# Kernel optimization log

Hardware: AMD Instinct MI355X
Metric: run time of the kernel (lower is better)

The kernel has to match this reference:

```python
import jax, jax.numpy as jnp
import numpy as np

FP8_MAX = 448.0   # max finite value of float8_e4m3fn
GROUP = 128       # quant group size (both act cols and weight blocks)


def fp8_roundtrip(v):
    # Round-to-nearest onto the fp8 e4m3fn grid, back to f32.
    return v.astype(jnp.float8_e4m3fn).astype(jnp.float32)


def setup_inputs() -> dict:
    key = jax.random.key(0)
    k1, k2, k3 = jax.random.split(key, 3)
    M, H = 8192, 4096
    x = jax.random.normal(k1, (M, 2 * H), dtype=jnp.float32)
    # weight: rand -> fp8 grid (stored as f32 values lying exactly on fp8 grid)
    w_q = fp8_roundtrip(jax.random.uniform(k2, (H, H), dtype=jnp.float32))
    # per-(128,128)-block weight scales
    wscale = jax.random.uniform(k3, (H // GROUP, H // GROUP), dtype=jnp.float32)
    return {"x": x, "w_q": w_q, "wscale": wscale}


def reference(x, w_q, wscale):
    H = x.shape[-1] // 2
    # SiluAndMul: silu(gate) * up
    y = jax.nn.silu(x[:, :H]) * x[:, H:]            # [M, H]
    M = y.shape[0]
    # --- activation group quant, group shape (1, 128) ---
    g = y.reshape(M, H // GROUP, GROUP)
    amax = jnp.max(jnp.abs(g), axis=-1, keepdims=True)
    scale = jnp.maximum(amax, 1e-12) / FP8_MAX      # [M, H/128, 1]
    q = fp8_roundtrip(g / scale)                    # fp8-grid values
    y_dq = (q * scale).reshape(M, H)                # dequantized activation
    # --- weight block dequant, block shape (128, 128) ---
    nk, nn = H // GROUP, H // GROUP
    w_dq = (w_q.reshape(nk, GROUP, nn, GROUP) * wscale[:, None, :, None]).reshape(H, H)
    # block-fp8 linear: out[m, n] = sum_k y_dq[m, k] * w_dq[k, n]
    return y_dq @ w_dq
```

## Files before the change

kernel.cpp:

```cpp
#include <hip/hip_runtime.h>
#include <hip/hip_fp8.h>

#define MDIM 8192
#define HDIM 4096

typedef float f32x4 __attribute__((ext_vector_type(4)));
typedef long i64;

__device__ inline void gload_lds16(const void* g, void* l) {
  __builtin_amdgcn_global_load_lds(
      (const __attribute__((address_space(1))) void*)g,
      (__attribute__((address_space(3))) void*)l, 16, 0, 0);
}

__global__ __launch_bounds__(256) void silu_quant_kernel(
    const float* __restrict__ x, unsigned char* __restrict__ q,
    float* __restrict__ st) {
  const int m = blockIdx.x;
  const int t = threadIdx.x;
  const int g = t >> 3;
  const int i = t & 7;
  const float* xr = x + (size_t)m * (2 * HDIM);

  float v[16];
  float amax = 0.f;
#pragma unroll
  for (int j = 0; j < 4; ++j) {
    const int off = g * 128 + j * 32 + i * 4;
    f32x4 gate = *(const f32x4*)(xr + off);
    f32x4 up = *(const f32x4*)(xr + HDIM + off);
#pragma unroll
    for (int c = 0; c < 4; ++c) {
      float gg = gate[c];
      float s = gg / (1.f + expf(-gg));
      float val = s * up[c];
      v[j * 4 + c] = val;
      amax = fmaxf(amax, fabsf(val));
    }
  }
#pragma unroll
  for (int d = 1; d < 8; d <<= 1) amax = fmaxf(amax, __shfl_xor(amax, d, 64));
  const float scale = fmaxf(amax, 1e-12f) / 448.0f;

#pragma unroll
  for (int j = 0; j < 4; ++j) {
    unsigned int pk = 0;
#pragma unroll
    for (int c = 0; c < 4; ++c) {
      __hip_fp8_e4m3 qv(v[j * 4 + c] / scale);
      pk |= ((unsigned int)qv.__x) << (8 * c);
    }
    *(unsigned int*)(q + (size_t)m * HDIM + g * 128 + j * 32 + i * 4) = pk;
  }
  if (i == 0) st[(size_t)g * MDIM + m] = scale;
}

__global__ __launch_bounds__(256) void wconv_kernel(
    const float* __restrict__ w, unsigned char* __restrict__ wt) {
  __shared__ __align__(16) unsigned char tile[64 * 68];
  const int t = threadIdx.x;
  const int n0 = (blockIdx.x & 63) * 64;
  const int k0 = (blockIdx.x >> 6) * 64;
  {
    const int r = t >> 4;
    const int c4 = (t & 15) << 2;
#pragma unroll
    for (int j = 0; j < 4; ++j) {
      const int kr = r + j * 16;
      f32x4 vv = *(const f32x4*)(w + (size_t)(k0 + kr) * HDIM + n0 + c4);
      unsigned int pk = 0;
#pragma unroll
      for (int c = 0; c < 4; ++c) {
        __hip_fp8_e4m3 qv(vv[c]);
        pk |= ((unsigned int)qv.__x) << (8 * c);
      }
      *(unsigned int*)(tile + kr * 68 + c4) = pk;
    }
  }
  __syncthreads();
  {
    const int n = t >> 4;
    const int k4 = (t & 15) << 2;
#pragma unroll
    for (int j = 0; j < 4; ++j) {
      const int nn = n + j * 16;
      unsigned int pk = 0;
#pragma unroll
      for (int c = 0; c < 4; ++c)
        pk |= ((unsigned int)tile[(k4 + c) * 68 + nn]) << (8 * c);
      *(unsigned int*)(wt + (size_t)(n0 + nn) * HDIM + k0 + k4) = pk;
    }
  }
}

__global__ __launch_bounds__(256, 2) void gemm_fp8_kernel(
    const unsigned char* __restrict__ Aq,
    const unsigned char* __restrict__ Bt,
    const float* __restrict__ st,
    const float* __restrict__ wsc,
    float* __restrict__ out) {
  __shared__ __align__(16) unsigned char As[128 * 128];
  __shared__ __align__(16) unsigned char Bs[128 * 128];
  __shared__ __align__(16) float sas[128];

  const int t = threadIdx.x;
  const int ntile = blockIdx.x & 31;
  const int mtile = blockIdx.x >> 5;
  const int m0 = mtile * 128, n0 = ntile * 128;

  const int l = t & 63, wid = t >> 6;
  const int wm = wid >> 1, wn = wid & 1;
  const int lrow = l & 15, lhi = l >> 4;

  f32x4 acc[4][4];
#pragma unroll
  for (int a = 0; a < 4; ++a)
#pragma unroll
    for (int b = 0; b < 4; ++b) acc[a][b] = (f32x4){0.f, 0.f, 0.f, 0.f};

  const int sr = t >> 3;
  const int skc = (t & 7) ^ (sr & 7);

  for (int kb = 0; kb < 32; ++kb) {
    __syncthreads();
    const int kbase = kb * 128 + skc * 16;
#pragma unroll
    for (int p = 0; p < 4; ++p) {
      const int row = sr + p * 32;
      gload_lds16(Aq + (size_t)(m0 + row) * HDIM + kbase, As + (p * 256 + t) * 16);
      gload_lds16(Bt + (size_t)(n0 + row) * HDIM + kbase, Bs + (p * 256 + t) * 16);
    }
    if (t < 128) sas[t] = st[(size_t)kb * MDIM + m0 + t];
    __syncthreads();

    const float sw = wsc[kb * 32 + ntile];

    f32x4 blk[4][4];
#pragma unroll
    for (int kk = 0; kk < 4; ++kk) {
      const int kbyte = kk * 32 + lhi * 8;
      const int chunk = (((kbyte >> 4) ^ (lrow & 7)) << 4) + (kbyte & 15);
      i64 af[4], bf[4];
#pragma unroll
      for (int mi = 0; mi < 4; ++mi) {
        const int row = wm * 64 + mi * 16 + lrow;
        af[mi] = *(const i64*)(As + row * 128 + chunk);
      }
#pragma unroll
      for (int ni = 0; ni < 4; ++ni) {
        const int row = wn * 64 + ni * 16 + lrow;
        bf[ni] = *(const i64*)(Bs + row * 128 + chunk);
      }
#pragma unroll
      for (int mi = 0; mi < 4; ++mi)
#pragma unroll
        for (int ni = 0; ni < 4; ++ni) {
          f32x4 cin = (kk == 0) ? (f32x4){0.f, 0.f, 0.f, 0.f} : blk[mi][ni];
          blk[mi][ni] =
              __builtin_amdgcn_mfma_f32_16x16x32_fp8_fp8(af[mi], bf[ni], cin, 0, 0, 0);
        }
    }
#pragma unroll
    for (int mi = 0; mi < 4; ++mi) {
      f32x4 sa = *(const f32x4*)(sas + wm * 64 + mi * 16 + lhi * 4);
      f32x4 sm;
#pragma unroll
      for (int r = 0; r < 4; ++r) sm[r] = sa[r] * sw;
#pragma unroll
      for (int ni = 0; ni < 4; ++ni)
#pragma unroll
        for (int r = 0; r < 4; ++r)
          acc[mi][ni][r] = fmaf(blk[mi][ni][r], sm[r], acc[mi][ni][r]);
    }
  }

#pragma unroll
  for (int mi = 0; mi < 4; ++mi)
#pragma unroll
    for (int r = 0; r < 4; ++r) {
      const int grow = m0 + wm * 64 + mi * 16 + lhi * 4 + r;
      float* orow = out + (size_t)grow * HDIM + n0 + wn * 64 + lrow;
#pragma unroll
      for (int ni = 0; ni < 4; ++ni) orow[ni * 16] = acc[mi][ni][r];
    }
}

extern "C" void kernel_launch(void* const* d_in, const int* in_sizes, int n_in,
                              void* d_out, int out_size, void* d_ws, size_t ws_size,
                              hipStream_t stream) {
  const float* x = (const float*)d_in[0];
  const float* wq = (const float*)d_in[1];
  const float* wsc = (const float*)d_in[2];
  float* out = (float*)d_out;

  unsigned char* q = (unsigned char*)d_ws;
  unsigned char* wt = q + (size_t)MDIM * HDIM;
  float* st = (float*)(wt + (size_t)HDIM * HDIM);

  silu_quant_kernel<<<MDIM, 256, 0, stream>>>(x, q, st);
  wconv_kernel<<<(HDIM / 64) * (HDIM / 64), 256, 0, stream>>>(wq, wt);
  gemm_fp8_kernel<<<(MDIM / 128) * (HDIM / 128), 256, 0, stream>>>(q, wt, st, wsc, out);
}
```

Baseline: 341.6 us.

## Switch GEMM to bf16 with pre-dequantized operands and double-buffered 256x256 tiles

Activations are now quantized to the fp8 grid, dequantized, and stored as bf16. Weights are pre-multiplied by their block scales and stored as bf16. This removes the per-k-block scale epilogue from the GEMM, which becomes a plain bf16 MFMA kernel with 256x256 tiles, 512 threads, double-buffered LDS staging and a swizzled block order. The trade-off is that bf16 MFMA has lower throughput than fp8 and the operands take twice the memory traffic. Rounding the dequantized values to bf16 may also add a small error against the reference.

```diff
diff --git a/kernel.cpp b/kernel.cpp
--- a/kernel.cpp
+++ b/kernel.cpp
@@ -1,11 +1,14 @@
 #include <hip/hip_runtime.h>
 #include <hip/hip_fp8.h>
+#include <hip/hip_bf16.h>
 
 #define MDIM 8192
 #define HDIM 4096
+#define NKT 64
 
 typedef float f32x4 __attribute__((ext_vector_type(4)));
-typedef long i64;
+typedef short bf16x8 __attribute__((ext_vector_type(8)));
+typedef unsigned short u16x4 __attribute__((ext_vector_type(4)));
 
 __device__ inline void gload_lds16(const void* g, void* l) {
   __builtin_amdgcn_global_load_lds(
@@ -13,9 +16,13 @@
       (__attribute__((address_space(3))) void*)l, 16, 0, 0);
 }
 
+__device__ inline unsigned short f2bf(float f) {
+  __hip_bfloat16 h = __float2bfloat16(f);
+  return *reinterpret_cast<unsigned short*>(&h);
+}
+
 __global__ __launch_bounds__(256) void silu_quant_kernel(
-    const float* __restrict__ x, unsigned char* __restrict__ q,
-    float* __restrict__ st) {
+    const float* __restrict__ x, unsigned short* __restrict__ yb) {
   const int m = blockIdx.x;
   const int t = threadIdx.x;
   const int g = t >> 3;
@@ -44,23 +51,24 @@
 
 #pragma unroll
   for (int j = 0; j < 4; ++j) {
-    unsigned int pk = 0;
+    u16x4 pk;
 #pragma unroll
     for (int c = 0; c < 4; ++c) {
       __hip_fp8_e4m3 qv(v[j * 4 + c] / scale);
-      pk |= ((unsigned int)qv.__x) << (8 * c);
-    }
-    *(unsigned int*)(q + (size_t)m * HDIM + g * 128 + j * 32 + i * 4) = pk;
-  }
-  if (i == 0) st[(size_t)g * MDIM + m] = scale;
+      pk[c] = f2bf((float)qv * scale);
+    }
+    *(u16x4*)(yb + (size_t)m * HDIM + g * 128 + j * 32 + i * 4) = pk;
+  }
 }
 
 __global__ __launch_bounds__(256) void wconv_kernel(
-    const float* __restrict__ w, unsigned char* __restrict__ wt) {
-  __shared__ __align__(16) unsigned char tile[64 * 68];
+    const float* __restrict__ w, const float* __restrict__ wsc,
+    unsigned short* __restrict__ wt) {
+  __shared__ unsigned short tile[64][66];
   const int t = threadIdx.x;
   const int n0 = (blockIdx.x & 63) * 64;
   const int k0 = (blockIdx.x >> 6) * 64;
+  const float ws = wsc[(k0 >> 7) * 32 + (n0 >> 7)];
   {
     const int r = t >> 4;
     const int c4 = (t & 15) << 2;
@@ -68,13 +76,8 @@
     for (int j = 0; j < 4; ++j) {
       const int kr = r + j * 16;
       f32x4 vv = *(const f32x4*)(w + (size_t)(k0 + kr) * HDIM + n0 + c4);
-      unsigned int pk = 0;
-#pragma unroll
-      for (int c = 0; c < 4; ++c) {
-        __hip_fp8_e4m3 qv(vv[c]);
-        pk |= ((unsigned int)qv.__x) << (8 * c);
-      }
-      *(unsigned int*)(tile + kr * 68 + c4) = pk;
+#pragma unroll
+      for (int c = 0; c < 4; ++c) tile[kr][c4 + c] = f2bf(vv[c] * ws);
     }
   }
   __syncthreads();
@@ -84,105 +87,123 @@
 #pragma unroll
     for (int j = 0; j < 4; ++j) {
       const int nn = n + j * 16;
-      unsigned int pk = 0;
-#pragma unroll
-      for (int c = 0; c < 4; ++c)
-        pk |= ((unsigned int)tile[(k4 + c) * 68 + nn]) << (8 * c);
-      *(unsigned int*)(wt + (size_t)(n0 + nn) * HDIM + k0 + k4) = pk;
-    }
-  }
-}
-
-__global__ __launch_bounds__(256, 2) void gemm_fp8_kernel(
-    const unsigned char* __restrict__ Aq,
-    const unsigned char* __restrict__ Bt,
-    const float* __restrict__ st,
-    const float* __restrict__ wsc,
+      u16x4 pk;
+#pragma unroll
+      for (int c = 0; c < 4; ++c) pk[c] = tile[k4 + c][nn];
+      *(u16x4*)(wt + (size_t)(n0 + nn) * HDIM + k0 + k4) = pk;
+    }
+  }
+}
+
+#define SBAR do { __builtin_amdgcn_sched_barrier(0); __builtin_amdgcn_s_barrier(); __builtin_amdgcn_sched_barrier(0); } while (0)
+#define VMW0 asm volatile("s_waitcnt vmcnt(0)" ::: "memory")
+#define LGKM0 asm volatile("s_waitcnt lgkmcnt(0)" ::: "memory")
+
+#define STAGE_UNIT(nx, kt, u) do {                                          \
+    const __hip_bfloat16* gsrc;  unsigned char* ldst;                       \
+    if ((u) == 0)      { gsrc = A + (size_t)(m0 + r0) * HDIM;       ldst = As[nx]; }          \
+    else if ((u) == 1) { gsrc = B + (size_t)(n0 + r0) * HDIM;       ldst = Bs[nx]; }          \
+    else if ((u) == 2) { gsrc = A + (size_t)(m0 + 128 + r0) * HDIM; ldst = As[nx] + 16384; }  \
+    else               { gsrc = B + (size_t)(n0 + 128 + r0) * HDIM; ldst = Bs[nx] + 16384; }  \
+    gsrc += (kt) * 64 + cst * 8;                                            \
+    gload_lds16(gsrc, ldst + t * 16);                                       \
+    gload_lds16(gsrc + (size_t)64 * HDIM, ldst + 8192 + t * 16);            \
+  } while (0)
+
+#define STAGE_ALL(nx, kt) do {                                              \
+    STAGE_UNIT(nx, kt, 0); STAGE_UNIT(nx, kt, 1);                           \
+    STAGE_UNIT(nx, kt, 2); STAGE_UNIT(nx, kt, 3);                           \
+    __builtin_amdgcn_sched_barrier(0);                                      \
+  } while (0)
+
+#define RD_A(cur, mh) do { _Pragma("unroll") for (int mi = 0; mi < 4; ++mi) { \
+    const int row = wm * 128 + (mh) * 64 + mi * 16 + lrow;                    \
+    _Pragma("unroll") for (int kk = 0; kk < 2; ++kk)                          \
+      afr[mi][kk] = *(const bf16x8*)(As[cur] + row * 128 + (((kk * 4 + lhi) ^ rx) * 16)); \
+  } } while (0)
+
+#define RD_B(cur, nh) do { _Pragma("unroll") for (int ni = 0; ni < 2; ++ni) { \
+    const int row = wn * 64 + (nh) * 32 + ni * 16 + lrow;                     \
+    _Pragma("unroll") for (int kk = 0; kk < 2; ++kk)                          \
+      bfr[nh][ni][kk] = *(const bf16x8*)(Bs[cur] + row * 128 + (((kk * 4 + lhi) ^ rx) * 16)); \
+  } } while (0)
+
+#define MFMA16(mh, nh) do { _Pragma("unroll") for (int kk = 0; kk < 2; ++kk)  \
+    _Pragma("unroll") for (int mi = 0; mi < 4; ++mi)                          \
+      _Pragma("unroll") for (int ni = 0; ni < 2; ++ni)                        \
+        acc[(mh) * 4 + mi][(nh) * 2 + ni] = __builtin_amdgcn_mfma_f32_16x16x32_bf16( \
+            afr[mi][kk], bfr[nh][ni][kk], acc[(mh) * 4 + mi][(nh) * 2 + ni], 0, 0, 0); \
+  } while (0)
+
+#define COMPUTE(cur) do {                                                    \
+    RD_A(cur, 0); RD_B(cur, 0); RD_B(cur, 1);                                \
+    __builtin_amdgcn_s_setprio(1);                                           \
+    MFMA16(0, 0); MFMA16(0, 1);                                              \
+    __builtin_amdgcn_s_setprio(0);                                           \
+    RD_A(cur, 1);                                                            \
+    __builtin_amdgcn_s_setprio(1);                                           \
+    MFMA16(1, 0); MFMA16(1, 1);                                              \
+    __builtin_amdgcn_s_setprio(0);                                           \
+  } while (0)
+
+__global__ __launch_bounds__(512, 2) void gemm_bf16_kernel(
+    const __hip_bfloat16* __restrict__ A,
+    const __hip_bfloat16* __restrict__ B,
     float* __restrict__ out) {
-  __shared__ __align__(16) unsigned char As[128 * 128];
-  __shared__ __align__(16) unsigned char Bs[128 * 128];
-  __shared__ __align__(16) float sas[128];
+  __shared__ __align__(16) unsigned char As[2][32768];
+  __shared__ __align__(16) unsigned char Bs[2][32768];
+
+  const int bid = blockIdx.x;
+  const int swz = (bid & 7) * 64 + (bid >> 3);
+  const int m0 = (swz & 31) * 256;
+  const int n0 = (swz >> 5) * 256;
 
   const int t = threadIdx.x;
-  const int ntile = blockIdx.x & 31;
-  const int mtile = blockIdx.x >> 5;
-  const int m0 = mtile * 128, n0 = ntile * 128;
-
   const int l = t & 63, wid = t >> 6;
-  const int wm = wid >> 1, wn = wid & 1;
+  const int wm = wid >> 2, wn = wid & 3;
   const int lrow = l & 15, lhi = l >> 4;
-
-  f32x4 acc[4][4];
-#pragma unroll
-  for (int a = 0; a < 4; ++a)
+  const int rx = lrow & 7;
+
+  const int r0 = t >> 3;
+  const int cst = (t & 7) ^ (r0 & 7);
+
+  f32x4 acc[8][4];
+#pragma unroll
+  for (int a = 0; a < 8; ++a)
 #pragma unroll
     for (int b = 0; b < 4; ++b) acc[a][b] = (f32x4){0.f, 0.f, 0.f, 0.f};
-
-  const int sr = t >> 3;
-  const int skc = (t & 7) ^ (sr & 7);
-
-  for (int kb = 0; kb < 32; ++kb) {
-    __syncthreads();
-    const int kbase = kb * 128 + skc * 16;
-#pragma unroll
-    for (int p = 0; p < 4; ++p) {
-      const int row = sr + p * 32;
-      gload_lds16(Aq + (size_t)(m0 + row) * HDIM + kbase, As + (p * 256 + t) * 16);
-      gload_lds16(Bt + (size_t)(n0 + row) * HDIM + kbase, Bs + (p * 256 + t) * 16);
-    }
-    if (t < 128) sas[t] = st[(size_t)kb * MDIM + m0 + t];
-    __syncthreads();
-
-    const float sw = wsc[kb * 32 + ntile];
-
-    f32x4 blk[4][4];
-#pragma unroll
-    for (int kk = 0; kk < 4; ++kk) {
-      const int kbyte = kk * 32 + lhi * 8;
-      const int chunk = (((kbyte >> 4) ^ (lrow & 7)) << 4) + (kbyte & 15);
-      i64 af[4], bf[4];
-#pragma unroll
-      for (int mi = 0; mi < 4; ++mi) {
-        const int row = wm * 64 + mi * 16 + lrow;
-        af[mi] = *(const i64*)(As + row * 128 + chunk);
+  bf16x8 afr[4][2], bfr[2][2][2];
+
+  STAGE_ALL(0, 0);
+  VMW0;
+  SBAR;
+
+  int cur = 0;
+  for (int kt = 0; kt < NKT - 1; ++kt) {
+    const int nx = cur ^ 1;
+    STAGE_ALL(nx, kt + 1);
+    COMPUTE(cur);
+    VMW0;
+    LGKM0;
+    SBAR;
+    cur = nx;
+  }
+  COMPUTE(cur);
+
+#pragma unroll
+  for (int a = 0; a < 8; ++a) {
+    const int moff = (a >> 2) * 64 + (a & 3) * 16;
+#pragma unroll
+    for (int r = 0; r < 4; ++r) {
+      const int grow = m0 + wm * 128 + moff + lhi * 4 + r;
+      float* orow = out + (size_t)grow * HDIM + n0 + wn * 64 + lrow;
+#pragma unroll
+      for (int b = 0; b < 4; ++b) {
+        const int coff = (b >> 1) * 32 + (b & 1) * 16;
+        orow[coff] = acc[a][b][r];
       }
-#pragma unroll
-      for (int ni = 0; ni < 4; ++ni) {
-        const int row = wn * 64 + ni * 16 + lrow;
-        bf[ni] = *(const i64*)(Bs + row * 128 + chunk);
-      }
-#pragma unroll
-      for (int mi = 0; mi < 4; ++mi)
-#pragma unroll
-        for (int ni = 0; ni < 4; ++ni) {
-          f32x4 cin = (kk == 0) ? (f32x4){0.f, 0.f, 0.f, 0.f} : blk[mi][ni];
-          blk[mi][ni] =
-              __builtin_amdgcn_mfma_f32_16x16x32_fp8_fp8(af[mi], bf[ni], cin, 0, 0, 0);
-        }
-    }
-#pragma unroll
-    for (int mi = 0; mi < 4; ++mi) {
-      f32x4 sa = *(const f32x4*)(sas + wm * 64 + mi * 16 + lhi * 4);
-      f32x4 sm;
-#pragma unroll
-      for (int r = 0; r < 4; ++r) sm[r] = sa[r] * sw;
-#pragma unroll
-      for (int ni = 0; ni < 4; ++ni)
-#pragma unroll
-        for (int r = 0; r < 4; ++r)
-          acc[mi][ni][r] = fmaf(blk[mi][ni][r], sm[r], acc[mi][ni][r]);
-    }
-  }
-
-#pragma unroll
-  for (int mi = 0; mi < 4; ++mi)
-#pragma unroll
-    for (int r = 0; r < 4; ++r) {
-      const int grow = m0 + wm * 64 + mi * 16 + lhi * 4 + r;
-      float* orow = out + (size_t)grow * HDIM + n0 + wn * 64 + lrow;
-#pragma unroll
-      for (int ni = 0; ni < 4; ++ni) orow[ni * 16] = acc[mi][ni][r];
-    }
+    }
+  }
 }
 
 extern "C" void kernel_launch(void* const* d_in, const int* in_sizes, int n_in,
@@ -193,11 +214,11 @@
   const float* wsc = (const float*)d_in[2];
   float* out = (float*)d_out;
 
-  unsigned char* q = (unsigned char*)d_ws;
-  unsigned char* wt = q + (size_t)MDIM * HDIM;
-  float* st = (float*)(wt + (size_t)HDIM * HDIM);
-
-  silu_quant_kernel<<<MDIM, 256, 0, stream>>>(x, q, st);
-  wconv_kernel<<<(HDIM / 64) * (HDIM / 64), 256, 0, stream>>>(wq, wt);
-  gemm_fp8_kernel<<<(MDIM / 128) * (HDIM / 128), 256, 0, stream>>>(q, wt, st, wsc, out);
-}
+  unsigned short* yb = (unsigned short*)d_ws;
+  unsigned short* wt = yb + (size_t)MDIM * HDIM;
+
+  silu_quant_kernel<<<MDIM, 256, 0, stream>>>(x, yb);
+  wconv_kernel<<<(HDIM / 64) * (HDIM / 64), 256, 0, stream>>>(wq, wsc, wt);
+  gemm_bf16_kernel<<<(MDIM / 256) * (HDIM / 256), 512, 0, stream>>>(
+      (const __hip_bfloat16*)yb, (const __hip_bfloat16*)wt, out);
+}
```

Result: slower. 363.2 us (+6.3%).
